# Kernel tuning notes

Measured on AMD Instinct MI355X. Metric: run time of the kernel, lower is better.

The kernel has to match this reference:

```python
import jax, jax.numpy as jnp
import numpy as np

HQ, HKV, D = 16, 2, 128   # num_heads_q, num_heads_kv, head_dim
G = HQ // HKV             # q heads per kv head (repeat_interleave factor)


def setup_inputs() -> dict:
    key = jax.random.key(0)
    ks = jax.random.split(key, 6)
    B, T, C = 2, 2048, 2048
    def w(k, shape):
        return jax.random.normal(k, shape, jnp.float32) * (1.0 / np.sqrt(shape[0]).astype(np.float32))
    x = jax.random.normal(ks[0], (B, T, C), jnp.float32)
    Wq = w(ks[1], (C, HQ * D))
    Wk = w(ks[2], (C, HKV * D))
    Wv = w(ks[3], (C, HKV * D))
    Wo = w(ks[4], (HQ * D, C))
    Wg = w(ks[5], (C, HQ))
    # causal mask: True where attention is disallowed (j > i)
    mask = jnp.triu(jnp.ones((T, T), dtype=bool), k=1)[None, None]  # (1,1,T,T)
    return {"x": x, "mask": mask, "Wq": Wq, "Wk": Wk, "Wv": Wv, "Wo": Wo, "Wg": Wg}


def reference(x, mask, Wq, Wk, Wv, Wo, Wg):
    B, T, C = x.shape
    # repeat_interleave(G, dim=heads) means q head h uses kv head h // G,
    # so group q heads as (HKV, G) instead of materializing repeated K/V.
    q = (x @ Wq).reshape(B, T, HKV, G, D).transpose(0, 2, 3, 1, 4)  # (B,HKV,G,T,D)
    k = (x @ Wk).reshape(B, T, HKV, D).transpose(0, 2, 1, 3)        # (B,HKV,T,D)
    v = (x @ Wv).reshape(B, T, HKV, D).transpose(0, 2, 1, 3)        # (B,HKV,T,D)
    scale = jnp.float32(1.0 / np.sqrt(D))
    scores = jnp.einsum('bkgtd,bksd->bkgts', q, k) * scale          # (B,HKV,G,T,T)
    scores = jnp.where(mask[:, None], jnp.float32(-1e9), scores)    # causal fill
    attn = jax.nn.softmax(scores, axis=-1)
    # post-softmax sigmoid gate, one scalar per (batch, q-head, query token)
    gates = jax.nn.sigmoid(x @ Wg)                                   # (B,T,HQ)
    gates = gates.transpose(0, 2, 1).reshape(B, HKV, G, T)           # (B,HKV,G,T)
    out = jnp.einsum('bkgts,bksd->btkgd', attn * gates[..., None], v)
    out = out.reshape(B, T, HQ * D)
    return out @ Wo
```

## Files before the change

### kernel.cpp

```cpp
#include <hip/hip_runtime.h>
#include <hip/hip_bf16.h>
#include <math.h>

#define HQ 16
#define HKV 2
#define D 128
#define B_SZ 2
#define T_SZ 2048
#define C_SZ 2048
#define QKVN 2688

#define C_Q 0.12753102f
#define C_G 1.44269504f

typedef __attribute__((ext_vector_type(8))) short short8;
typedef __attribute__((ext_vector_type(4))) float floatx4;

static __device__ __forceinline__ float fexp2(float x) {
    return __builtin_amdgcn_exp2f(x);
}

static __device__ __forceinline__ unsigned short f2b(float f) {
    union { float f; unsigned u; } x; x.f = f;
    return (unsigned short)((x.u + 0x7fffu + ((x.u >> 16) & 1u)) >> 16);
}

static __device__ __forceinline__ unsigned int pk2(float a, float b) {
    float2 t; t.x = a; t.y = b;
    __hip_bfloat162 h = __float22bfloat162_rn(t);
    return *(unsigned int*)&h;
}

static __device__ __forceinline__ void load_lds16(const void* g, void* l) {
    __builtin_amdgcn_global_load_lds(
        (const __attribute__((address_space(1))) void*)g,
        (__attribute__((address_space(3))) void*)l,
        16, 0, 0);
}

static __device__ __forceinline__ void tr32(
    const float* __restrict__ in, unsigned short* __restrict__ out,
    int R, int Cc, float premul, int bx, int by, float (*t)[33])
{
    const int bc = bx * 32, br = by * 32;
    const int tid = threadIdx.x;
    const int r = tid >> 3, c4 = (tid & 7) * 4;
    float4 v = *(const float4*)(in + (size_t)(br + r) * Cc + bc + c4);
    t[r][c4 + 0] = v.x; t[r][c4 + 1] = v.y; t[r][c4 + 2] = v.z; t[r][c4 + 3] = v.w;
    __syncthreads();
    ushort4 o;
    o.x = f2b(t[c4 + 0][r] * premul); o.y = f2b(t[c4 + 1][r] * premul);
    o.z = f2b(t[c4 + 2][r] * premul); o.w = f2b(t[c4 + 3][r] * premul);
    *(ushort4*)(out + (size_t)(bc + r) * R + br + c4) = o;
}

__global__ __launch_bounds__(256) void prep_kernel(
    const float* __restrict__ x,  const float* __restrict__ Wq,
    const float* __restrict__ Wk, const float* __restrict__ Wv,
    const float* __restrict__ Wo, const float* __restrict__ Wg,
    unsigned short* __restrict__ xb, unsigned short* __restrict__ Wqkvt,
    unsigned short* __restrict__ Wot)
{
    __shared__ float t[32][33];
    const int bid = blockIdx.x;
    const int tid = threadIdx.x;
    if (bid < 4096) {
        int i = bid * 2048 + tid * 8;
        float4 a = *(const float4*)(x + i);
        float4 b = *(const float4*)(x + i + 4);
        ushort4 o0, o1;
        o0.x = f2b(a.x); o0.y = f2b(a.y); o0.z = f2b(a.z); o0.w = f2b(a.w);
        o1.x = f2b(b.x); o1.y = f2b(b.y); o1.z = f2b(b.z); o1.w = f2b(b.w);
        *(ushort4*)(xb + i) = o0;
        *(ushort4*)(xb + i + 4) = o1;
    } else if (bid < 8192) {
        int n = bid - 4096;
        tr32(Wq, Wqkvt, C_SZ, HQ * D, C_Q, n & 63, n >> 6, t);
    } else if (bid < 8704) {
        int n = bid - 8192;
        tr32(Wk, Wqkvt + (size_t)(HQ * D) * C_SZ, C_SZ, HKV * D, 1.0f, n & 7, n >> 3, t);
    } else if (bid < 9216) {
        int n = bid - 8704;
        tr32(Wv, Wqkvt + (size_t)(HQ * D + HKV * D) * C_SZ, C_SZ, HKV * D, 1.0f, n & 7, n >> 3, t);
    } else if (bid < 13312) {
        int n = bid - 9216;
        tr32(Wo, Wot, HQ * D, C_SZ, 1.0f, n & 63, n >> 6, t);
    } else {
        int k = (bid - 13312) * 256 + tid;
        const float4* wr = (const float4*)(Wg + (size_t)k * 16);
        float4 w0 = wr[0], w1 = wr[1], w2 = wr[2], w3 = wr[3];
        float w[16] = {w0.x, w0.y, w0.z, w0.w, w1.x, w1.y, w1.z, w1.w,
                       w2.x, w2.y, w2.z, w2.w, w3.x, w3.y, w3.z, w3.w};
        unsigned short* out = Wqkvt + (size_t)(HQ * D + 2 * HKV * D) * C_SZ;
        #pragma unroll
        for (int h = 0; h < 16; ++h)
            out[(size_t)h * C_SZ + k] = f2b(w[h] * C_G);
    }
}

template<int BM>
__global__ __launch_bounds__(512, 2) void gemm8p(
    const unsigned short* __restrict__ A, const unsigned short* __restrict__ Bt,
    float* __restrict__ Cf, unsigned short* __restrict__ Cb,
    unsigned short* __restrict__ Vt, int Nreal, int K, int out_bf16)
{
    constexpr int MT = BM / 32;
    constexpr int MH = MT / 2;
    constexpr int LA = BM / 128;
    constexpr int AUNIT = (BM / 2) * 64;
    constexpr int BUNIT = 8192;
    constexpr int BUF = 2 * AUNIT + 2 * BUNIT;
    constexpr int VM = LA + 4;
    __shared__ __align__(16) unsigned short SM[2][BUF];

    const int tid = threadIdx.x;
    const int lane = tid & 63, wave = tid >> 6;
    const int l15 = lane & 15, quad = lane >> 4;
    const int wm = wave >> 2, wn = wave & 3;
    const int NT = K >> 6;

    const int nwg = (int)(gridDim.x * gridDim.y);
    int flat = (int)(blockIdx.y * gridDim.x + blockIdx.x);
    const int cpx = nwg >> 3;
    flat = (flat & 7) * cpx + (flat >> 3);
    const int bm0 = (flat / (int)gridDim.x) * BM;
    const int bn0 = (flat % (int)gridDim.x) * 256;

    const int rr = tid >> 3;
    const int cb8 = ((tid & 7) ^ (rr & 7)) << 3;
    unsigned aoff[2][LA], boff[2][2];
    #pragma unroll
    for (int mh = 0; mh < 2; ++mh)
        #pragma unroll
        for (int j = 0; j < LA; ++j) {
            int row_l = j * 64 + rr;
            int grow;
            if (BM == 256) grow = bm0 + (row_l >> 6) * 128 + mh * 64 + (row_l & 63);
            else           grow = bm0 + (row_l >> 5) * 64  + mh * 32 + (row_l & 31);
            aoff[mh][j] = (unsigned)((grow * K + cb8) * 2);
        }
    #pragma unroll
    for (int nh = 0; nh < 2; ++nh)
        #pragma unroll
        for (int j = 0; j < 2; ++j) {
            int row_l = j * 64 + rr;
            int gnr = bn0 + (row_l >> 5) * 64 + nh * 32 + (row_l & 31);
            boff[nh][j] = (unsigned)((gnr * K + cb8) * 2);
        }

    floatx4 zero = {0.f, 0.f, 0.f, 0.f};
    floatx4 acc[MT][4];
    #pragma unroll
    for (int i = 0; i < MT; ++i)
        #pragma unroll
        for (int j = 0; j < 4; ++j) acc[i][j] = zero;

    auto STAGE_A = [&](int b, int mh, int t) {
        #pragma unroll
        for (int j = 0; j < LA; ++j)
            load_lds16((const char*)A + aoff[mh][j] + (size_t)t * 128,
                       &SM[b][mh * AUNIT + (j * 512 + wave * 64) * 8]);
    };
    auto STAGE_B = [&](int b, int nh, int t) {
        #pragma unroll
        for (int j = 0; j < 2; ++j)
            load_lds16((const char*)Bt + boff[nh][j] + (size_t)t * 128,
                       &SM[b][2 * AUNIT + nh * BUNIT + (j * 512 + wave * 64) * 8]);
    };

    short8 fa[MH][2], fb[4][2];
    auto RD_A = [&](int b, int mh) {
        const unsigned short* Sa = &SM[b][mh * AUNIT];
        #pragma unroll
        for (int i = 0; i < MH; ++i) {
            const int row_l = wm * (BM / 4) + i * 16 + l15;
            #pragma unroll
            for (int kk = 0; kk < 2; ++kk)
                fa[i][kk] = *(const short8*)&Sa[row_l * 64 +
                    ((((kk << 2) + quad) ^ (l15 & 7)) << 3)];
        }
    };
    auto RD_Bh = [&](int b, int nh) {
        const unsigned short* Sb = &SM[b][2 * AUNIT + nh * BUNIT];
        #pragma unroll
        for (int s = 0; s < 2; ++s) {
            const int row_l = wn * 32 + s * 16 + l15;
            #pragma unroll
            for (int kk = 0; kk < 2; ++kk)
                fb[nh * 2 + s][kk] = *(const short8*)&Sb[row_l * 64 +
                    ((((kk << 2) + quad) ^ (l15 & 7)) << 3)];
        }
    };
    auto MMQ = [&](int mh, int nh) {
        __builtin_amdgcn_s_setprio(1);
        #pragma unroll
        for (int i = 0; i < MH; ++i)
            #pragma unroll
            for (int s = 0; s < 2; ++s)
                #pragma unroll
                for (int kk = 0; kk < 2; ++kk)
                    acc[mh * MH + i][nh * 2 + s] = __builtin_amdgcn_mfma_f32_16x16x32_bf16(
                        fa[i][kk], fb[nh * 2 + s][kk], acc[mh * MH + i][nh * 2 + s], 0, 0, 0);
        __builtin_amdgcn_s_setprio(0);
    };

    STAGE_A(0, 0, 0); STAGE_B(0, 0, 0); STAGE_B(0, 1, 0); STAGE_A(0, 1, 0);
    if (NT > 1) { STAGE_A(1, 0, 1); STAGE_B(1, 0, 1); STAGE_B(1, 1, 1); }
    asm volatile("s_waitcnt vmcnt(%0)" :: "n"(VM));
    __builtin_amdgcn_s_barrier();

    #pragma unroll 2
    for (int t = 0; t < NT; ++t) {
        const int b = t & 1;
        RD_A(b, 0); RD_Bh(b, 0);
        if (t + 1 < NT) STAGE_A(b ^ 1, 1, t + 1);
        asm volatile("s_waitcnt lgkmcnt(8)");
        __builtin_amdgcn_s_barrier();
        asm volatile("s_waitcnt lgkmcnt(0)");
        MMQ(0, 0);
        __builtin_amdgcn_s_barrier();
        RD_Bh(b, 1);
        if (t + 2 < NT) STAGE_A(b, 0, t + 2);
        __builtin_amdgcn_s_barrier();
        asm volatile("s_waitcnt lgkmcnt(0)");
        MMQ(0, 1);
        __builtin_amdgcn_s_barrier();
        RD_A(b, 1);
        if (t + 2 < NT) STAGE_B(b, 0, t + 2);
        __builtin_amdgcn_s_barrier();
        asm volatile("s_waitcnt lgkmcnt(0)");
        MMQ(1, 1);
        __builtin_amdgcn_s_barrier();
        if (t + 2 < NT) {
            STAGE_B(b, 1, t + 2);
            asm volatile("s_waitcnt vmcnt(%0)" :: "n"(VM));
        } else {
            asm volatile("s_waitcnt vmcnt(0)");
        }
        __builtin_amdgcn_s_barrier();
        MMQ(1, 0);
        __builtin_amdgcn_s_barrier();
    }

    if (BM == 256 && Vt != nullptr && bn0 == 2304) {
        unsigned short (*Ct)[264] = (unsigned short(*)[264])SM;
        const int bb = bm0 >> 11;
        const int tl = bm0 & 2047;
        #pragma unroll
        for (int v = 0; v < 4; ++v) {
            __syncthreads();
            if (wn == v) {
                #pragma unroll
                for (int mt = 0; mt < MT; ++mt)
                    #pragma unroll
                    for (int nt = 0; nt < 4; ++nt)
                        #pragma unroll
                        for (int r = 0; r < 4; ++r)
                            Ct[nt * 16 + l15][wm * (BM / 2) + mt * 16 + quad * 4 + r] =
                                f2b(acc[mt][nt][r]);
            }
            __syncthreads();
            int row = tid >> 3, c0 = (tid & 7) * 32;
            unsigned short* dst = Vt + ((size_t)bb * (HKV * D) + v * 64 + row) * T_SZ
                                     + tl + c0;
            const unsigned short* src = &Ct[row][c0];
            short8 s0 = *(const short8*)(src + 0);
            short8 s1 = *(const short8*)(src + 8);
            short8 s2 = *(const short8*)(src + 16);
            short8 s3 = *(const short8*)(src + 24);
            *(short8*)(dst + 0)  = s0; *(short8*)(dst + 8)  = s1;
            *(short8*)(dst + 16) = s2; *(short8*)(dst + 24) = s3;
        }
        return;
    }

    #pragma unroll
    for (int mt = 0; mt < MT; ++mt)
        #pragma unroll
        for (int nt = 0; nt < 4; ++nt) {
            const int n = bn0 + wn * 64 + nt * 16 + l15;
            if (n < Nreal) {
                #pragma unroll
                for (int r = 0; r < 4; ++r) {
                    const int m = bm0 + wm * (BM / 2) + mt * 16 + quad * 4 + r;
                    if (out_bf16) Cb[(size_t)m * Nreal + n] = f2b(acc[mt][nt][r]);
                    else          Cf[(size_t)m * Nreal + n] = acc[mt][nt][r];
                }
            }
        }
}

__global__ __launch_bounds__(512, 4) void attn_mfma(
    const unsigned short* __restrict__ QKV, const unsigned short* __restrict__ Vt,
    unsigned short* __restrict__ Ob)
{
    __shared__ __align__(16) unsigned short SMEM[2 * 8192 + 2 * 8192 + 128 * 40];
    unsigned short* Ks = SMEM;
    unsigned short* Vs = SMEM + 16384;
    unsigned short* Ps = SMEM + 32768;
    unsigned short* Lo = SMEM;

    const int bh = blockIdx.x;
    const int j = (int)gridDim.y - 1 - (int)blockIdx.y;
    const int b = bh >> 4, h = bh & 15, kvh = h >> 3;
    const int tid = threadIdx.x;
    const int lane = tid & 63, w = tid >> 6;
    const int l15 = lane & 15, quad = lane >> 4;
    const int q_local = w * 16 + l15;
    const int qw  = j * 2 + (q_local >> 6);
    const int qhi = j * 2 + 1;
    const float BIAS = 32.0f;

    short8 aq[4];
    {
        const unsigned short* qp = QKV + (size_t)(b * T_SZ + j * 128 + q_local) * QKVN
                                       + h * D + quad * 8;
        #pragma unroll
        for (int kd = 0; kd < 4; ++kd) aq[kd] = *(const short8*)(qp + kd * 32);
    }

    const unsigned short* kg[2];
    const unsigned short* vg[2];
    #pragma unroll
    for (int it = 0; it < 2; ++it) {
        int Bi = it * 512 + tid;
        int kr = Bi >> 4, kc = ((Bi & 15) ^ (kr & 15)) * 8;
        kg[it] = QKV + (size_t)(b * T_SZ + kr) * QKVN + HQ * D + kvh * D + kc;
        int vr = Bi >> 3, vc = ((Bi & 7) ^ (vr & 7)) * 8;
        vg[it] = Vt + (size_t)((b * HKV + kvh) * D + vr) * T_SZ + vc;
    }

    floatx4 zero = {0.f, 0.f, 0.f, 0.f};
    floatx4 oacc[8];
    #pragma unroll
    for (int dt = 0; dt < 8; ++dt) oacc[dt] = zero;
    float l_part = 0.f;

    auto STAGE = [&](int kt, int buf) {
        #pragma unroll
        for (int it = 0; it < 2; ++it) {
            load_lds16(kg[it] + (size_t)kt * 64 * QKVN,
                       &Ks[buf * 8192 + (it * 512 + w * 64) * 8]);
            load_lds16(vg[it] + kt * 64,
                       &Vs[buf * 8192 + (it * 512 + w * 64) * 8]);
        }
    };

    STAGE(0, 0);
    for (int kt = 0; kt <= qhi; ++kt) {
        const int cur = kt & 1;
        __syncthreads();
        if (kt < qhi) STAGE(kt + 1, cur ^ 1);
        if (kt > qw) continue;

        const unsigned short* Kc = Ks + cur * 8192;
        const unsigned short* Vc = Vs + cur * 8192;

        floatx4 sacc[4];
        #pragma unroll
        for (int nt = 0; nt < 4; ++nt) sacc[nt] = zero;
        #pragma unroll
        for (int kd = 0; kd < 4; ++kd)
            #pragma unroll
            for (int nt = 0; nt < 4; ++nt) {
                short8 ak = *(const short8*)&Kc[((nt * 16 + l15) * 16 + ((kd * 4 + quad) ^ l15)) * 8];
                sacc[nt] = __builtin_amdgcn_mfma_f32_16x16x32_bf16(ak, aq[kd], sacc[nt], 0, 0, 0);
            }

        const int qm = q_local & 63;
        const bool atq = (kt == qw);
        #pragma unroll
        for (int kk = 0; kk < 2; ++kk) {
            #pragma unroll
            for (int ntl = 0; ntl < 2; ++ntl) {
                const int nt = kk * 2 + ntl;
                float p[4];
                if (atq) {
                    #pragma unroll
                    for (int r = 0; r < 4; ++r) {
                        float e = fexp2(sacc[nt][r] - BIAS);
                        p[r] = (nt * 16 + quad * 4 + r > qm) ? 0.f : e;
                    }
                } else {
                    #pragma unroll
                    for (int r = 0; r < 4; ++r)
                        p[r] = fexp2(sacc[nt][r] - BIAS);
                }
                l_part += (p[0] + p[1]) + (p[2] + p[3]);
                uint2 pw;
                pw.x = pk2(p[0], p[1]);
                pw.y = pk2(p[2], p[3]);
                *(uint2*)&Ps[(w * 16 + l15) * 40 + ntl * 16 + quad * 4] = pw;
            }
            short8 bp = *(const short8*)&Ps[(w * 16 + l15) * 40 + quad * 8];
            #pragma unroll
            for (int dt = 0; dt < 8; ++dt) {
                short8 av = *(const short8*)&Vc[((dt * 16 + l15) * 8 + ((kk * 4 + quad) ^ (l15 & 7))) * 8];
                oacc[dt] = __builtin_amdgcn_mfma_f32_16x16x32_bf16(av, bp, oacc[dt], 0, 0, 0);
            }
        }
    }

    float l = l_part;
    l += __shfl_xor(l, 16);
    l += __shfl_xor(l, 32);

    __syncthreads();
    {
        int token = b * T_SZ + j * 128 + q_local;
        unsigned short gl = QKV[(size_t)token * QKVN + HQ * D + HKV * D * 2 + h];
        union { unsigned u; float f; } gx; gx.u = ((unsigned)gl) << 16;
        float g = 1.0f / (1.0f + fexp2(-gx.f));
        float f = g / l;
        #pragma unroll
        for (int dt = 0; dt < 8; ++dt) {
            uint2 ov;
            ov.x = pk2(oacc[dt][0] * f, oacc[dt][1] * f);
            ov.y = pk2(oacc[dt][2] * f, oacc[dt][3] * f);
            *(uint2*)&Lo[(size_t)q_local * 136 + dt * 16 + quad * 4] = ov;
        }
    }
    __syncthreads();
    {
        int row = tid >> 2, c0 = (tid & 3) * 32;
        size_t tok = (size_t)(b * T_SZ + j * 128 + row);
        unsigned short* op = Ob + tok * (HQ * D) + h * D + c0;
        const unsigned short* lp = &Lo[(size_t)row * 136 + c0];
        short8 v0 = *(const short8*)(lp + 0);
        short8 v1 = *(const short8*)(lp + 8);
        short8 v2 = *(const short8*)(lp + 16);
        short8 v3 = *(const short8*)(lp + 24);
        *(short8*)(op + 0)  = v0; *(short8*)(op + 8)  = v1;
        *(short8*)(op + 16) = v2; *(short8*)(op + 24) = v3;
    }
}

extern "C" void kernel_launch(void* const* d_in, const int* in_sizes, int n_in,
                              void* d_out, int out_size, void* d_ws, size_t ws_size,
                              hipStream_t stream) {
    const float* x  = (const float*)d_in[0];
    const float* Wq = (const float*)d_in[2];
    const float* Wk = (const float*)d_in[3];
    const float* Wv = (const float*)d_in[4];
    const float* Wo = (const float*)d_in[5];
    const float* Wg = (const float*)d_in[6];
    float* out = (float*)d_out;

    const size_t KB = 1ull << 10;
    char* p = (char*)d_ws;
    unsigned short* xb    = (unsigned short*)(p);
    unsigned short* Ob    = xb;
    unsigned short* Wqkvt = (unsigned short*)(p + 16384 * KB);
    unsigned short* Wot   = (unsigned short*)(p + 27136 * KB);
    unsigned short* QKV   = (unsigned short*)(p + 35328 * KB);
    unsigned short* Vt    = (unsigned short*)(p + 56832 * KB);
    const int BT = B_SZ * T_SZ;

    prep_kernel<<<dim3(13320), 256, 0, stream>>>(x, Wq, Wk, Wv, Wo, Wg, xb, Wqkvt, Wot);

    gemm8p<256><<<dim3(11, BT / 256), 512, 0, stream>>>(
        xb, Wqkvt, nullptr, QKV, Vt, QKVN, C_SZ, 1);

    attn_mfma<<<dim3(B_SZ * HQ, T_SZ / 128), 512, 0, stream>>>(QKV, Vt, Ob);

    gemm8p<128><<<dim3(8, BT / 128), 512, 0, stream>>>(
        Ob, Wot, out, nullptr, nullptr, C_SZ, HQ * D, 0);
}
```

Before: 280.7 us.

## Pair causal query tiles per attention block and enlarge prep transpose tiles

The attention kernel now launches half as many blocks. Each block processes two query tiles, j and 15-j, in sequence, so every block does the same causal work and the tail imbalance from uneven blocks goes away. The price is fewer blocks in flight (256), and the occupancy hint in the launch bounds is dropped. The weight transpose in the prep kernel moves from 32x32 to 64x64 tiles with wider 16-byte stores, which cuts the block count and the per-block overhead but uses more LDS per block.

```diff
diff --git a/kernel.cpp b/kernel.cpp
--- a/kernel.cpp
+++ b/kernel.cpp
@@ -38,20 +38,30 @@
         16, 0, 0);
 }
 
-static __device__ __forceinline__ void tr32(
+static __device__ __forceinline__ void tr64(
     const float* __restrict__ in, unsigned short* __restrict__ out,
-    int R, int Cc, float premul, int bx, int by, float (*t)[33])
+    int R, int Cc, float premul, int bx, int by, float (*ts)[65])
 {
-    const int bc = bx * 32, br = by * 32;
+    const int bc = bx * 64, br = by * 64;
     const int tid = threadIdx.x;
-    const int r = tid >> 3, c4 = (tid & 7) * 4;
-    float4 v = *(const float4*)(in + (size_t)(br + r) * Cc + bc + c4);
-    t[r][c4 + 0] = v.x; t[r][c4 + 1] = v.y; t[r][c4 + 2] = v.z; t[r][c4 + 3] = v.w;
+    const int r = tid >> 2, c0 = (tid & 3) * 16;
+    const float* ip = in + (size_t)(br + r) * Cc + bc + c0;
+    #pragma unroll
+    for (int k = 0; k < 4; ++k) {
+        float4 v = *(const float4*)(ip + k * 4);
+        ts[r][c0 + k * 4 + 0] = v.x; ts[r][c0 + k * 4 + 1] = v.y;
+        ts[r][c0 + k * 4 + 2] = v.z; ts[r][c0 + k * 4 + 3] = v.w;
+    }
     __syncthreads();
-    ushort4 o;
-    o.x = f2b(t[c4 + 0][r] * premul); o.y = f2b(t[c4 + 1][r] * premul);
-    o.z = f2b(t[c4 + 2][r] * premul); o.w = f2b(t[c4 + 3][r] * premul);
-    *(ushort4*)(out + (size_t)(bc + r) * R + br + c4) = o;
+    const int wr = tid >> 3, wc = (tid & 7) * 8;
+    #pragma unroll
+    for (int half = 0; half < 2; ++half) {
+        const int row = wr + half * 32;
+        union { unsigned short u[8]; short8 v; } o;
+        #pragma unroll
+        for (int jj = 0; jj < 8; ++jj) o.u[jj] = f2b(ts[wc + jj][row] * premul);
+        *(short8*)(out + (size_t)(bc + row) * R + br + wc) = o.v;
+    }
 }
 
 __global__ __launch_bounds__(256) void prep_kernel(
@@ -61,7 +71,7 @@
     unsigned short* __restrict__ xb, unsigned short* __restrict__ Wqkvt,
     unsigned short* __restrict__ Wot)
 {
-    __shared__ float t[32][33];
+    __shared__ float ts[64][65];
     const int bid = blockIdx.x;
     const int tid = threadIdx.x;
     if (bid < 4096) {
@@ -73,20 +83,20 @@
         o1.x = f2b(b.x); o1.y = f2b(b.y); o1.z = f2b(b.z); o1.w = f2b(b.w);
         *(ushort4*)(xb + i) = o0;
         *(ushort4*)(xb + i + 4) = o1;
-    } else if (bid < 8192) {
+    } else if (bid < 5120) {
         int n = bid - 4096;
-        tr32(Wq, Wqkvt, C_SZ, HQ * D, C_Q, n & 63, n >> 6, t);
-    } else if (bid < 8704) {
-        int n = bid - 8192;
-        tr32(Wk, Wqkvt + (size_t)(HQ * D) * C_SZ, C_SZ, HKV * D, 1.0f, n & 7, n >> 3, t);
-    } else if (bid < 9216) {
-        int n = bid - 8704;
-        tr32(Wv, Wqkvt + (size_t)(HQ * D + HKV * D) * C_SZ, C_SZ, HKV * D, 1.0f, n & 7, n >> 3, t);
-    } else if (bid < 13312) {
-        int n = bid - 9216;
-        tr32(Wo, Wot, HQ * D, C_SZ, 1.0f, n & 63, n >> 6, t);
+        tr64(Wq, Wqkvt, C_SZ, HQ * D, C_Q, n & 31, n >> 5, ts);
+    } else if (bid < 5248) {
+        int n = bid - 5120;
+        tr64(Wk, Wqkvt + (size_t)(HQ * D) * C_SZ, C_SZ, HKV * D, 1.0f, n & 3, n >> 2, ts);
+    } else if (bid < 5376) {
+        int n = bid - 5248;
+        tr64(Wv, Wqkvt + (size_t)(HQ * D + HKV * D) * C_SZ, C_SZ, HKV * D, 1.0f, n & 3, n >> 2, ts);
+    } else if (bid < 6400) {
+        int n = bid - 5376;
+        tr64(Wo, Wot, HQ * D, C_SZ, 1.0f, n & 31, n >> 5, ts);
     } else {
-        int k = (bid - 13312) * 256 + tid;
+        int k = (bid - 6400) * 256 + tid;
         const float4* wr = (const float4*)(Wg + (size_t)k * 16);
         float4 w0 = wr[0], w1 = wr[1], w2 = wr[2], w3 = wr[3];
         float w[16] = {w0.x, w0.y, w0.z, w0.w, w1.x, w1.y, w1.z, w1.w,
@@ -290,7 +300,7 @@
         }
 }
 
-__global__ __launch_bounds__(512, 4) void attn_mfma(
+__global__ __launch_bounds__(512) void attn_mfma(
     const unsigned short* __restrict__ QKV, const unsigned short* __restrict__ Vt,
     unsigned short* __restrict__ Ob)
 {
@@ -301,23 +311,14 @@
     unsigned short* Lo = SMEM;
 
     const int bh = blockIdx.x;
-    const int j = (int)gridDim.y - 1 - (int)blockIdx.y;
+    const int jA = (int)blockIdx.y;
+    const int jB = 15 - jA;
     const int b = bh >> 4, h = bh & 15, kvh = h >> 3;
     const int tid = threadIdx.x;
     const int lane = tid & 63, w = tid >> 6;
     const int l15 = lane & 15, quad = lane >> 4;
     const int q_local = w * 16 + l15;
-    const int qw  = j * 2 + (q_local >> 6);
-    const int qhi = j * 2 + 1;
     const float BIAS = 32.0f;
-
-    short8 aq[4];
-    {
-        const unsigned short* qp = QKV + (size_t)(b * T_SZ + j * 128 + q_local) * QKVN
-                                       + h * D + quad * 8;
-        #pragma unroll
-        for (int kd = 0; kd < 4; ++kd) aq[kd] = *(const short8*)(qp + kd * 32);
-    }
 
     const unsigned short* kg[2];
     const unsigned short* vg[2];
@@ -330,12 +331,6 @@
         vg[it] = Vt + (size_t)((b * HKV + kvh) * D + vr) * T_SZ + vc;
     }
 
-    floatx4 zero = {0.f, 0.f, 0.f, 0.f};
-    floatx4 oacc[8];
-    #pragma unroll
-    for (int dt = 0; dt < 8; ++dt) oacc[dt] = zero;
-    float l_part = 0.f;
-
     auto STAGE = [&](int kt, int buf) {
         #pragma unroll
         for (int it = 0; it < 2; ++it) {
@@ -346,92 +341,114 @@
         }
     };
 
-    STAGE(0, 0);
-    for (int kt = 0; kt <= qhi; ++kt) {
-        const int cur = kt & 1;
+    floatx4 zero = {0.f, 0.f, 0.f, 0.f};
+
+    for (int pass = 0; pass < 2; ++pass) {
+        const int j = pass ? jB : jA;
+        const int qw  = j * 2 + (q_local >> 6);
+        const int qhi = j * 2 + 1;
+
+        short8 aq[4];
+        {
+            const unsigned short* qp = QKV + (size_t)(b * T_SZ + j * 128 + q_local) * QKVN
+                                           + h * D + quad * 8;
+            #pragma unroll
+            for (int kd = 0; kd < 4; ++kd) aq[kd] = *(const short8*)(qp + kd * 32);
+        }
+
+        floatx4 oacc[8];
+        #pragma unroll
+        for (int dt = 0; dt < 8; ++dt) oacc[dt] = zero;
+        float l_part = 0.f;
+
         __syncthreads();
-        if (kt < qhi) STAGE(kt + 1, cur ^ 1);
-        if (kt > qw) continue;
-
-        const unsigned short* Kc = Ks + cur * 8192;
-        const unsigned short* Vc = Vs + cur * 8192;
-
-        floatx4 sacc[4];
-        #pragma unroll
-        for (int nt = 0; nt < 4; ++nt) sacc[nt] = zero;
-        #pragma unroll
-        for (int kd = 0; kd < 4; ++kd)
-            #pragma unroll
-            for (int nt = 0; nt < 4; ++nt) {
-                short8 ak = *(const short8*)&Kc[((nt * 16 + l15) * 16 + ((kd * 4 + quad) ^ l15)) * 8];
-                sacc[nt] = __builtin_amdgcn_mfma_f32_16x16x32_bf16(ak, aq[kd], sacc[nt], 0, 0, 0);
+        STAGE(0, 0);
+        for (int kt = 0; kt <= qhi; ++kt) {
+            const int cur = kt & 1;
+            __syncthreads();
+            if (kt < qhi) STAGE(kt + 1, cur ^ 1);
+            if (kt > qw) continue;
+
+            const unsigned short* Kc = Ks + cur * 8192;
+            const unsigned short* Vc = Vs + cur * 8192;
+
+            floatx4 sacc[4];
+            #pragma unroll
+            for (int nt = 0; nt < 4; ++nt) sacc[nt] = zero;
+            #pragma unroll
+            for (int kd = 0; kd < 4; ++kd)
+                #pragma unroll
+                for (int nt = 0; nt < 4; ++nt) {
+                    short8 ak = *(const short8*)&Kc[((nt * 16 + l15) * 16 + ((kd * 4 + quad) ^ l15)) * 8];
+                    sacc[nt] = __builtin_amdgcn_mfma_f32_16x16x32_bf16(ak, aq[kd], sacc[nt], 0, 0, 0);
+                }
+
+            const int qm = q_local & 63;
+            const bool atq = (kt == qw);
+            #pragma unroll
+            for (int kk = 0; kk < 2; ++kk) {
+                #pragma unroll
+                for (int ntl = 0; ntl < 2; ++ntl) {
+                    const int nt = kk * 2 + ntl;
+                    float p[4];
+                    if (atq) {
+                        #pragma unroll
+                        for (int r = 0; r < 4; ++r) {
+                            float e = fexp2(sacc[nt][r] - BIAS);
+                            p[r] = (nt * 16 + quad * 4 + r > qm) ? 0.f : e;
+                        }
+                    } else {
+                        #pragma unroll
+                        for (int r = 0; r < 4; ++r)
+                            p[r] = fexp2(sacc[nt][r] - BIAS);
+                    }
+                    l_part += (p[0] + p[1]) + (p[2] + p[3]);
+                    uint2 pw;
+                    pw.x = pk2(p[0], p[1]);
+                    pw.y = pk2(p[2], p[3]);
+                    *(uint2*)&Ps[(w * 16 + l15) * 40 + ntl * 16 + quad * 4] = pw;
+                }
+                short8 bp = *(const short8*)&Ps[(w * 16 + l15) * 40 + quad * 8];
+                #pragma unroll
+                for (int dt = 0; dt < 8; ++dt) {
+                    short8 av = *(const short8*)&Vc[((dt * 16 + l15) * 8 + ((kk * 4 + quad) ^ (l15 & 7))) * 8];
+                    oacc[dt] = __builtin_amdgcn_mfma_f32_16x16x32_bf16(av, bp, oacc[dt], 0, 0, 0);
+                }
             }
-
-        const int qm = q_local & 63;
-        const bool atq = (kt == qw);
-        #pragma unroll
-        for (int kk = 0; kk < 2; ++kk) {
-            #pragma unroll
-            for (int ntl = 0; ntl < 2; ++ntl) {
-                const int nt = kk * 2 + ntl;
-                float p[4];
-                if (atq) {
-                    #pragma unroll
-                    for (int r = 0; r < 4; ++r) {
-                        float e = fexp2(sacc[nt][r] - BIAS);
-                        p[r] = (nt * 16 + quad * 4 + r > qm) ? 0.f : e;
-                    }
-                } else {
-                    #pragma unroll
-                    for (int r = 0; r < 4; ++r)
-                        p[r] = fexp2(sacc[nt][r] - BIAS);
-                }
-                l_part += (p[0] + p[1]) + (p[2] + p[3]);
-                uint2 pw;
-                pw.x = pk2(p[0], p[1]);
-                pw.y = pk2(p[2], p[3]);
-                *(uint2*)&Ps[(w * 16 + l15) * 40 + ntl * 16 + quad * 4] = pw;
+        }
+
+        float l = l_part;
+        l += __shfl_xor(l, 16);
+        l += __shfl_xor(l, 32);
+
+        __syncthreads();
+        {
+            int token = b * T_SZ + j * 128 + q_local;
+            unsigned short gl = QKV[(size_t)token * QKVN + HQ * D + HKV * D * 2 + h];
+            union { unsigned u; float f; } gx; gx.u = ((unsigned)gl) << 16;
+            float g = 1.0f / (1.0f + fexp2(-gx.f));
+            float f = g / l;
+            #pragma unroll
+            for (int dt = 0; dt < 8; ++dt) {
+                uint2 ov;
+                ov.x = pk2(oacc[dt][0] * f, oacc[dt][1] * f);
+                ov.y = pk2(oacc[dt][2] * f, oacc[dt][3] * f);
+                *(uint2*)&Lo[(size_t)q_local * 136 + dt * 16 + quad * 4] = ov;
             }
-            short8 bp = *(const short8*)&Ps[(w * 16 + l15) * 40 + quad * 8];
-            #pragma unroll
-            for (int dt = 0; dt < 8; ++dt) {
-                short8 av = *(const short8*)&Vc[((dt * 16 + l15) * 8 + ((kk * 4 + quad) ^ (l15 & 7))) * 8];
-                oacc[dt] = __builtin_amdgcn_mfma_f32_16x16x32_bf16(av, bp, oacc[dt], 0, 0, 0);
-            }
-        }
-    }
-
-    float l = l_part;
-    l += __shfl_xor(l, 16);
-    l += __shfl_xor(l, 32);
-
-    __syncthreads();
-    {
-        int token = b * T_SZ + j * 128 + q_local;
-        unsigned short gl = QKV[(size_t)token * QKVN + HQ * D + HKV * D * 2 + h];
-        union { unsigned u; float f; } gx; gx.u = ((unsigned)gl) << 16;
-        float g = 1.0f / (1.0f + fexp2(-gx.f));
-        float f = g / l;
-        #pragma unroll
-        for (int dt = 0; dt < 8; ++dt) {
-            uint2 ov;
-            ov.x = pk2(oacc[dt][0] * f, oacc[dt][1] * f);
-            ov.y = pk2(oacc[dt][2] * f, oacc[dt][3] * f);
-            *(uint2*)&Lo[(size_t)q_local * 136 + dt * 16 + quad * 4] = ov;
-        }
-    }
-    __syncthreads();
-    {
-        int row = tid >> 2, c0 = (tid & 3) * 32;
-        size_t tok = (size_t)(b * T_SZ + j * 128 + row);
-        unsigned short* op = Ob + tok * (HQ * D) + h * D + c0;
-        const unsigned short* lp = &Lo[(size_t)row * 136 + c0];
-        short8 v0 = *(const short8*)(lp + 0);
-        short8 v1 = *(const short8*)(lp + 8);
-        short8 v2 = *(const short8*)(lp + 16);
-        short8 v3 = *(const short8*)(lp + 24);
-        *(short8*)(op + 0)  = v0; *(short8*)(op + 8)  = v1;
-        *(short8*)(op + 16) = v2; *(short8*)(op + 24) = v3;
+        }
+        __syncthreads();
+        {
+            int row = tid >> 2, c0 = (tid & 3) * 32;
+            size_t tok = (size_t)(b * T_SZ + j * 128 + row);
+            unsigned short* op = Ob + tok * (HQ * D) + h * D + c0;
+            const unsigned short* lp = &Lo[(size_t)row * 136 + c0];
+            short8 v0 = *(const short8*)(lp + 0);
+            short8 v1 = *(const short8*)(lp + 8);
+            short8 v2 = *(const short8*)(lp + 16);
+            short8 v3 = *(const short8*)(lp + 24);
+            *(short8*)(op + 0)  = v0; *(short8*)(op + 8)  = v1;
+            *(short8*)(op + 16) = v2; *(short8*)(op + 24) = v3;
+        }
     }
 }
 
@@ -456,12 +473,12 @@
     unsigned short* Vt    = (unsigned short*)(p + 56832 * KB);
     const int BT = B_SZ * T_SZ;
 
-    prep_kernel<<<dim3(13320), 256, 0, stream>>>(x, Wq, Wk, Wv, Wo, Wg, xb, Wqkvt, Wot);
+    prep_kernel<<<dim3(6408), 256, 0, stream>>>(x, Wq, Wk, Wv, Wo, Wg, xb, Wqkvt, Wot);
 
     gemm8p<256><<<dim3(11, BT / 256), 512, 0, stream>>>(
         xb, Wqkvt, nullptr, QKV, Vt, QKVN, C_SZ, 1);
 
-    attn_mfma<<<dim3(B_SZ * HQ, T_SZ / 128), 512, 0, stream>>>(QKV, Vt, Ob);
+    attn_mfma<<<dim3(B_SZ * HQ, 8), 512, 0, stream>>>(QKV, Vt, Ob);
 
     gemm8p<128><<<dim3(8, BT / 128), 512, 0, stream>>>(
         Ob, Wot, out, nullptr, nullptr, C_SZ, HQ * D, 0);
```

Result: no change. 282.0 us (+0.5%).
